# Performance work log

Hardware: AMD Instinct MI355X
Metric: run time of the kernel (lower is better)

## Reference

```python
import jax, jax.numpy as jnp
import numpy as np

D_MODEL = 1024
NHEAD = 16
HEAD_DIM = D_MODEL // NHEAD  # 64
SEQ = 2048
BATCH = 2


def setup_inputs() -> dict:
    key = jax.random.key(0)
    ks = jax.random.split(key, 11)
    s = 0.02  # weight init scale
    f32 = jnp.float32
    return {
        "query": jax.random.normal(ks[0], (SEQ, BATCH, D_MODEL), f32),
        "key": jax.random.normal(ks[1], (SEQ, BATCH, D_MODEL), f32),
        "value": jax.random.normal(ks[2], (SEQ, BATCH, D_MODEL), f32),
        "attn_mask": jnp.ones((SEQ, SEQ), jnp.int32),
        "Wq": jax.random.normal(ks[3], (D_MODEL, D_MODEL), f32) * s,
        "bq": jnp.zeros((D_MODEL,), f32),
        "Wk": jax.random.normal(ks[4], (D_MODEL, D_MODEL), f32) * s,
        "bk": jnp.zeros((D_MODEL,), f32),
        "Wv": jax.random.normal(ks[5], (D_MODEL, D_MODEL), f32) * s,
        "bv": jnp.zeros((D_MODEL,), f32),
        "Wo": jax.random.normal(ks[6], (D_MODEL, D_MODEL), f32) * s,
        "bo": jnp.zeros((D_MODEL,), f32),
    }


def reference(query, key, value, attn_mask, Wq, bq, Wk, bk, Wv, bv, Wo, bo):
    # query/key/value: [S, B, D] (seq-first, torch convention)
    S, B, D = query.shape
    H, Dh = NHEAD, D // NHEAD
    scale = 1.0 / np.float32(np.sqrt(Dh))

    def proj_heads(x, W, b):
        # Linear + split heads: [S,B,D] -> [H,B,S,Dh] (matches transpose(0,2))
        y = jnp.einsum('sbd,ed->sbe', x, W) + b
        return y.reshape(x.shape[0], B, H, Dh).transpose(2, 1, 0, 3)

    q = proj_heads(query, Wq, bq)   # [H,B,S,Dh]
    k = proj_heads(key, Wk, bk)     # [H,B,Sk,Dh]
    v = proj_heads(value, Wv, bv)   # [H,B,Sk,Dh]

    scores = jnp.einsum('hbqd,hbkd->hbqk', q, k) * scale  # [H,B,S,Sk]
    scores = jnp.where(attn_mask == 0, jnp.float32(-1e9), scores)
    attn_weights = jax.nn.softmax(scores, axis=-1)
    # dropout is identity in eval / p=0

    out = jnp.einsum('hbqk,hbkd->hbqd', attn_weights, v)  # [H,B,S,Dh]
    out = out.transpose(2, 1, 0, 3).reshape(S, B, D)
    out = jnp.einsum('sbd,ed->sbe', out, Wo) + bo
    return out, attn_weights
```

## Files before the change

kernel.cpp:

```cpp
#include <hip/hip_runtime.h>
#include <hip/hip_bf16.h>

#define DEVI __device__ __forceinline__

typedef __hip_bfloat16 bf16;
typedef __attribute__((ext_vector_type(8))) short bf16x8;
typedef __attribute__((ext_vector_type(4))) float f32x4;

constexpr int S  = 2048;
constexpr int B  = 2;
constexpr int D  = 1024;
constexpr int H  = 16;
constexpr int DH = 64;
constexpr int M  = S * B;
constexpr int K  = D;

DEVI f32x4 mfma16(bf16x8 a, bf16x8 b, f32x4 c) {
  return __builtin_amdgcn_mfma_f32_16x16x32_bf16(a, b, c, 0, 0, 0);
}

DEVI void gload16(const bf16* g, bf16* l) {
  __builtin_amdgcn_global_load_lds(
      (const __attribute__((address_space(1))) void*)g,
      (__attribute__((address_space(3))) void*)l, 16, 0, 0);
}

DEVI void cvt8_store(bf16* dst, float4 a, float4 b) {
  alignas(16) bf16 t[8];
  t[0] = __float2bfloat16(a.x); t[1] = __float2bfloat16(a.y);
  t[2] = __float2bfloat16(a.z); t[3] = __float2bfloat16(a.w);
  t[4] = __float2bfloat16(b.x); t[5] = __float2bfloat16(b.y);
  t[6] = __float2bfloat16(b.z); t[7] = __float2bfloat16(b.w);
  *(bf16x8*)dst = *(const bf16x8*)t;
}

__global__ __launch_bounds__(256)
void prep_k(const float* __restrict__ q, const float* __restrict__ k,
            const float* __restrict__ v,
            const float* __restrict__ Wq, const float* __restrict__ Wk,
            const float* __restrict__ Wv, const float* __restrict__ Wo,
            bf16* __restrict__ qb, bf16* __restrict__ kb, bf16* __restrict__ vb,
            bf16* __restrict__ wqb, bf16* __restrict__ wkb,
            bf16* __restrict__ wvb, bf16* __restrict__ wob) {
  int bid = blockIdx.x;
  const float* src; bf16* dst; int off;
  if      (bid < 2048) { src = q;  dst = qb;  off = bid; }
  else if (bid < 4096) { src = k;  dst = kb;  off = bid - 2048; }
  else if (bid < 6144) { src = v;  dst = vb;  off = bid - 4096; }
  else if (bid < 6656) { src = Wq; dst = wqb; off = bid - 6144; }
  else if (bid < 7168) { src = Wk; dst = wkb; off = bid - 6656; }
  else if (bid < 7680) { src = Wv; dst = wvb; off = bid - 7168; }
  else                 { src = Wo; dst = wob; off = bid - 7680; }
  size_t base = (size_t)off * 2048 + threadIdx.x * 8;
  float4 a = *(const float4*)&src[base];
  float4 c = *(const float4*)&src[base + 4];
  cvt8_store(&dst[base], a, c);
}

__global__ __launch_bounds__(256) void maskbits_k(const int* __restrict__ mask,
                                                  unsigned long long* __restrict__ bits) {
  int idx = blockIdx.x * 256 + threadIdx.x;
  int m = mask[idx];
  unsigned long long b = __ballot(m != 0);
  if ((threadIdx.x & 63) == 0) bits[idx >> 6] = b;
}

__global__ __launch_bounds__(64)
void rowfull_k(const unsigned long long* __restrict__ bits, unsigned* __restrict__ allq) {
  int g = blockIdx.x;
  int lane = threadIdx.x;
  bool ok = true;
  #pragma unroll
  for (int i = 0; i < 16; ++i)
    ok &= (bits[(size_t)g * 1024 + i * 64 + lane] == ~0ull);
  unsigned long long b = __ballot(ok);
  if (lane == 0) allq[g] = (b == ~0ull) ? 1u : 0u;
}

__global__ __launch_bounds__(256)
void gemm_qkv(const bf16* __restrict__ qb, const bf16* __restrict__ kb,
              const bf16* __restrict__ vb,
              const bf16* __restrict__ wqb, const bf16* __restrict__ wkb,
              const bf16* __restrict__ wvb,
              const float* __restrict__ bqp, const float* __restrict__ bkp,
              const float* __restrict__ bvp,
              bf16* __restrict__ qh, bf16* __restrict__ kh, bf16* __restrict__ vh) {
  __shared__ bf16 lA[128 * 64];
  __shared__ bf16 lB[128 * 64];

  const int z = blockIdx.z;
  const bf16* A     = (z == 0) ? qb  : (z == 1) ? kb  : vb;
  const bf16* W     = (z == 0) ? wqb : (z == 1) ? wkb : wvb;
  const float* bias = (z == 0) ? bqp : (z == 1) ? bkp : bvp;
  bf16* obf         = (z == 0) ? qh  : (z == 1) ? kh  : vh;

  const int tid  = threadIdx.x;
  const int lane = tid & 63;
  const int wave = tid >> 6;
  const int m0   = blockIdx.x * 128;
  const int n0   = blockIdx.y * 128;
  const int wm   = (wave >> 1) * 64;
  const int wn   = (wave & 1) * 64;
  const int lr   = lane & 15;
  const int lg   = lane >> 4;

  const int srow = wave * 32 + (lane >> 3);
  const int scol = (lane & 7) * 8;
  const bf16* gA = A + (size_t)(m0 + srow) * K + scol;
  const bf16* gB = W + (size_t)(n0 + srow) * K + scol;
  bf16* sA = &lA[srow * 64 + scol];
  bf16* sB = &lB[srow * 64 + scol];

  f32x4 acc[4][4] = {};

  for (int k0 = 0; k0 < K; k0 += 64) {
    __syncthreads();
    #pragma unroll
    for (int c = 0; c < 4; ++c) {
      gload16(gA + k0 + (size_t)c * 8 * K, sA + c * 8 * 64);
      gload16(gB + k0 + (size_t)c * 8 * K, sB + c * 8 * 64);
    }
    __syncthreads();

    bf16x8 af[4][2], bfv[4][2];
    #pragma unroll
    for (int f = 0; f < 4; ++f)
      #pragma unroll
      for (int kk = 0; kk < 2; ++kk) {
        af[f][kk]  = *(const bf16x8*)&lA[(wm + f * 16 + lr) * 64 + kk * 32 + lg * 8];
        bfv[f][kk] = *(const bf16x8*)&lB[(wn + f * 16 + lr) * 64 + kk * 32 + lg * 8];
      }
    #pragma unroll
    for (int kk = 0; kk < 2; ++kk)
      #pragma unroll
      for (int i = 0; i < 4; ++i)
        #pragma unroll
        for (int j = 0; j < 4; ++j)
          acc[i][j] = mfma16(af[i][kk], bfv[j][kk], acc[i][j]);
  }

  #pragma unroll
  for (int j = 0; j < 4; ++j) {
    int gcol = n0 + wn + j * 16 + lr;
    float bv = bias[gcol];
    int h = gcol >> 6, dh = gcol & 63;
    #pragma unroll
    for (int i = 0; i < 4; ++i) {
      #pragma unroll
      for (int r = 0; r < 4; ++r) {
        int grow = m0 + wm + i * 16 + lg * 4 + r;
        float v = acc[i][j][r] + bv;
        int s = grow >> 1, b = grow & 1;
        obf[(((size_t)(h * 2 + b) * S + s) * 64 + dh)] = __float2bfloat16(v);
      }
    }
  }
}

__global__ __launch_bounds__(256)
void transpose_v(const bf16* __restrict__ vh, bf16* __restrict__ vt) {
  __shared__ bf16 lt[64 * 72];
  const int hb = blockIdx.y;
  const int s0 = blockIdx.x * 64;
  const int tid = threadIdx.x;
  const int row = tid >> 3;
  const int c8  = (tid & 7) * 8;

  const bf16* src = vh + ((size_t)hb * S + s0) * 64;
  #pragma unroll
  for (int p = 0; p < 2; ++p) {
    int r = row + p * 32;
    *(float4*)&lt[r * 72 + c8] = *(const float4*)&src[(size_t)r * 64 + c8];
  }
  __syncthreads();

  bf16* dst = vt + (size_t)hb * DH * S + s0;
  #pragma unroll
  for (int p = 0; p < 2; ++p) {
    int dh = row + p * 32;
    alignas(16) bf16 tmp[8];
    #pragma unroll
    for (int kk = 0; kk < 8; ++kk) tmp[kk] = lt[(c8 + kk) * 72 + dh];
    *(bf16x8*)&dst[(size_t)dh * S + c8] = *(const bf16x8*)tmp;
  }
}

__global__ __launch_bounds__(256)
void gemm_out(const bf16* __restrict__ A, const bf16* __restrict__ W,
              const float* __restrict__ bias, float* __restrict__ of32) {
  __shared__ bf16 lA[128 * 64];
  __shared__ bf16 lB[128 * 64];

  const int tid  = threadIdx.x;
  const int lane = tid & 63;
  const int wave = tid >> 6;
  const int m0   = blockIdx.x * 128;
  const int n0   = blockIdx.y * 128;
  const int wm   = (wave >> 1) * 64;
  const int wn   = (wave & 1) * 64;
  const int lr   = lane & 15;
  const int lg   = lane >> 4;

  const int srow = wave * 32 + (lane >> 3);
  const int scol = (lane & 7) * 8;
  const bf16* gA = A + (size_t)(m0 + srow) * K + scol;
  const bf16* gB = W + (size_t)(n0 + srow) * K + scol;
  bf16* sA = &lA[srow * 64 + scol];
  bf16* sB = &lB[srow * 64 + scol];

  f32x4 acc[4][4] = {};

  for (int k0 = 0; k0 < K; k0 += 64) {
    __syncthreads();
    #pragma unroll
    for (int c = 0; c < 4; ++c) {
      gload16(gA + k0 + (size_t)c * 8 * K, sA + c * 8 * 64);
      gload16(gB + k0 + (size_t)c * 8 * K, sB + c * 8 * 64);
    }
    __syncthreads();

    bf16x8 af[4][2], bfv[4][2];
    #pragma unroll
    for (int f = 0; f < 4; ++f)
      #pragma unroll
      for (int kk = 0; kk < 2; ++kk) {
        af[f][kk]  = *(const bf16x8*)&lA[(wm + f * 16 + lr) * 64 + kk * 32 + lg * 8];
        bfv[f][kk] = *(const bf16x8*)&lB[(wn + f * 16 + lr) * 64 + kk * 32 + lg * 8];
      }
    #pragma unroll
    for (int kk = 0; kk < 2; ++kk)
      #pragma unroll
      for (int i = 0; i < 4; ++i)
        #pragma unroll
        for (int j = 0; j < 4; ++j)
          acc[i][j] = mfma16(af[i][kk], bfv[j][kk], acc[i][j]);
  }

  #pragma unroll
  for (int j = 0; j < 4; ++j) {
    int gcol = n0 + wn + j * 16 + lr;
    float bv = bias[gcol];
    #pragma unroll
    for (int i = 0; i < 4; ++i)
      #pragma unroll
      for (int r = 0; r < 4; ++r) {
        int grow = m0 + wm + i * 16 + lg * 4 + r;
        of32[(size_t)grow * D + gcol] = acc[i][j][r] + bv;
      }
  }
}


DEVI void stage_tile(const bf16* gbase, size_t gstride, int tid, bf16* lbuf) {
  #pragma unroll
  for (int i = 0; i < 2; ++i) {
    int slot = i * 256 + tid;
    int row  = slot >> 3;
    int colb = (slot & 7) * 16;
    int scolb = colb ^ ((row & 7) << 4);
    gload16(gbase + (size_t)row * gstride + (scolb >> 1), &lbuf[slot * 8]);
  }
}

DEVI bf16x8 frag_swz(const bf16* lbuf, int r, int colb) {
  int a = r * 128 + (colb ^ ((r & 7) << 4));
  return *(const bf16x8*)((const char*)lbuf + a);
}

__global__ __launch_bounds__(256)
void attn_k(const bf16* __restrict__ qh, const bf16* __restrict__ kh,
            const bf16* __restrict__ vt, const unsigned long long* __restrict__ mbits,
            const unsigned* __restrict__ allq,
            float* __restrict__ wout, bf16* __restrict__ aob) {
  __shared__ bf16 lK[2][64 * 64];
  __shared__ bf16 lV[2][64 * 64];
  __shared__ bf16 lW[4][16 * 40];

  const int tid = threadIdx.x, lane = tid & 63, wave = tid >> 6;
  const int hb = blockIdx.y;
  const int q0 = blockIdx.x * 64 + wave * 16;
  const bf16* Kb = kh + (size_t)hb * S * DH;
  const bf16* Vb = vt + (size_t)hb * DH * S;
  const bf16* Qb = qh + (size_t)hb * S * DH;
  const int lr = lane & 15, lg = lane >> 4;
  const float scale2 = 0.125f * 1.44269504089f;

  const bool fullmask = (allq[q0 >> 5] != 0u);

  bf16x8 qf[2];
  #pragma unroll
  for (int kk = 0; kk < 2; ++kk)
    qf[kk] = *(const bf16x8*)&Qb[(size_t)(q0 + lr) * DH + kk * 32 + lg * 8];

  float lrow[4] = {0.f, 0.f, 0.f, 0.f};

  stage_tile(Kb, DH, tid, lK[0]);
  for (int t = 0; t < 32; ++t) {
    int cur = t & 1;
    __syncthreads();
    if (t + 1 < 32) stage_tile(Kb + (size_t)(t + 1) * 64 * DH, DH, tid, lK[cur ^ 1]);

    f32x4 sa[4];
    #pragma unroll
    for (int c = 0; c < 4; ++c) {
      bf16x8 k0v = frag_swz(lK[cur], c * 16 + lr, lg * 16);
      bf16x8 k1v = frag_swz(lK[cur], c * 16 + lr, 64 + lg * 16);
      f32x4 z = {0.f, 0.f, 0.f, 0.f};
      z = mfma16(qf[0], k0v, z);
      sa[c] = mfma16(qf[1], k1v, z);
    }
    #pragma unroll
    for (int j = 0; j < 4; ++j) {
      float sv[4];
      #pragma unroll
      for (int c = 0; c < 4; ++c) sv[c] = sa[c][j] * scale2;
      if (!fullmask) {
        unsigned long long mw = mbits[(size_t)(q0 + lg * 4 + j) * 32 + t];
        #pragma unroll
        for (int c = 0; c < 4; ++c)
          sv[c] = ((mw >> (c * 16 + lr)) & 1ull) ? sv[c] : -1e9f;
      }
      lrow[j] += __builtin_amdgcn_exp2f(sv[0]) + __builtin_amdgcn_exp2f(sv[1])
               + __builtin_amdgcn_exp2f(sv[2]) + __builtin_amdgcn_exp2f(sv[3]);
    }
  }
  #pragma unroll
  for (int j = 0; j < 4; ++j) {
    float l = lrow[j];
    #pragma unroll
    for (int off = 1; off < 16; off <<= 1) l += __shfl_xor(l, off, 16);
    lrow[j] = 1.0f / l;
  }

  f32x4 oacc[4] = {};
  __syncthreads();
  stage_tile(Kb, DH, tid, lK[0]);
  stage_tile(Vb, S, tid, lV[0]);
  for (int t = 0; t < 32; ++t) {
    int cur = t & 1;
    __syncthreads();
    if (t + 1 < 32) {
      stage_tile(Kb + (size_t)(t + 1) * 64 * DH, DH, tid, lK[cur ^ 1]);
      stage_tile(Vb + (size_t)(t + 1) * 64, S, tid, lV[cur ^ 1]);
    }

    f32x4 sa[4];
    #pragma unroll
    for (int c = 0; c < 4; ++c) {
      bf16x8 k0v = frag_swz(lK[cur], c * 16 + lr, lg * 16);
      bf16x8 k1v = frag_swz(lK[cur], c * 16 + lr, 64 + lg * 16);
      f32x4 z = {0.f, 0.f, 0.f, 0.f};
      z = mfma16(qf[0], k0v, z);
      sa[c] = mfma16(qf[1], k1v, z);
    }

    #pragma unroll
    for (int u = 0; u < 2; ++u) {
      #pragma unroll
      for (int cc = 0; cc < 2; ++cc) {
        int c = u * 2 + cc;
        int cb = c * 16 + lr;
        #pragma unroll
        for (int j = 0; j < 4; ++j) {
          float sv = sa[c][j] * scale2;
          if (!fullmask) {
            unsigned long long mw = mbits[(size_t)(q0 + lg * 4 + j) * 32 + t];
            sv = ((mw >> cb) & 1ull) ? sv : -1e9f;
          }
          float w = __builtin_amdgcn_exp2f(sv) * lrow[j];
          int row = lg * 4 + j;
          wout[(size_t)(hb * S + q0 + row) * S + t * 64 + cb] = w;
          lW[wave][row * 40 + cc * 16 + lr] = __float2bfloat16(w);
        }
      }
      bf16x8 pa = *(const bf16x8*)&lW[wave][lr * 40 + lg * 8];
      #pragma unroll
      for (int nf = 0; nf < 4; ++nf) {
        bf16x8 vb = frag_swz(lV[cur], nf * 16 + lr, u * 64 + lg * 16);
        oacc[nf] = mfma16(pa, vb, oacc[nf]);
      }
    }
  }

  int h = hb >> 1, b = hb & 1;
  #pragma unroll
  for (int nf = 0; nf < 4; ++nf)
    #pragma unroll
    for (int r = 0; r < 4; ++r) {
      int sq = q0 + lg * 4 + r;
      int d  = h * 64 + nf * 16 + lr;
      aob[(size_t)(sq * 2 + b) * D + d] = __float2bfloat16(oacc[nf][r]);
    }
}

extern "C" void kernel_launch(void* const* d_in, const int* in_sizes, int n_in,
                              void* d_out, int out_size, void* d_ws, size_t ws_size,
                              hipStream_t stream) {
  const float* q    = (const float*)d_in[0];
  const float* k    = (const float*)d_in[1];
  const float* v    = (const float*)d_in[2];
  const int*   mask = (const int*)d_in[3];
  const float* Wq   = (const float*)d_in[4];
  const float* bq   = (const float*)d_in[5];
  const float* Wk   = (const float*)d_in[6];
  const float* bk   = (const float*)d_in[7];
  const float* Wv   = (const float*)d_in[8];
  const float* bv   = (const float*)d_in[9];
  const float* Wo   = (const float*)d_in[10];
  const float* bo   = (const float*)d_in[11];

  char* ws = (char*)d_ws;
  bf16* qh  = (bf16*)(ws);
  bf16* kh  = (bf16*)(ws + ((size_t)8  << 20));
  bf16* vt  = (bf16*)(ws + ((size_t)16 << 20));
  bf16* qbf = (bf16*)(ws + ((size_t)24 << 20));
  bf16* kbf = (bf16*)(ws + ((size_t)32 << 20));
  bf16* vbf = (bf16*)(ws + ((size_t)40 << 20));
  bf16* wqb = (bf16*)(ws + ((size_t)48 << 20));
  bf16* wkb = (bf16*)(ws + ((size_t)50 << 20));
  bf16* wvb = (bf16*)(ws + ((size_t)52 << 20));
  bf16* wob = (bf16*)(ws + ((size_t)54 << 20));
  unsigned long long* mbits =
      (unsigned long long*)(ws + ((size_t)56 << 20));
  unsigned* allq = (unsigned*)(ws + ((size_t)56 << 20) + (512 << 10));
  bf16* vh  = (bf16*)(ws + ((size_t)57 << 20));
  bf16* aob = qbf;

  float* outp = (float*)d_out;
  float* wout = outp + (size_t)M * D;

  prep_k<<<8192, 256, 0, stream>>>(q, k, v, Wq, Wk, Wv, Wo,
                                   qbf, kbf, vbf, wqb, wkb, wvb, wob);
  maskbits_k<<<dim3((S * S) / 256), 256, 0, stream>>>(mask, mbits);
  rowfull_k<<<64, 64, 0, stream>>>(mbits, allq);

  dim3 gq(M / 128, D / 128, 3);
  gemm_qkv<<<gq, 256, 0, stream>>>(qbf, kbf, vbf, wqb, wkb, wvb, bq, bk, bv,
                                   qh, kh, vh);

  dim3 gt(S / 64, H * B);
  transpose_v<<<gt, 256, 0, stream>>>(vh, vt);

  dim3 ga(S / 64, H * B);
  attn_k<<<ga, 256, 0, stream>>>(qh, kh, vt, mbits, allq, wout, aob);

  dim3 gg(M / 128, D / 128);
  gemm_out<<<gg, 256, 0, stream>>>(aob, wob, bo, outp);
}
```

Before: 312.0 us.

## Split attention pass-two into full-mask fast path with finer vmcnt barriers

Mask-fullness is now computed per 64-row query block instead of per 32 rows, so the whole block shares one uniform branch. In the full-mask case the second attention pass uses a specialised loop. It drops the per-element mask lookup and replaces __syncthreads with explicit s_waitcnt vmcnt plus s_barrier placed after compute, so the next tile's K/V loads can overlap the current tile's work. The hand-written vmcnt(16) count relies on the exact number of outstanding loads per stage, which is a correctness risk if that count differs.

```diff
diff --git a/kernel.cpp b/kernel.cpp
--- a/kernel.cpp
+++ b/kernel.cpp
@@ -71,8 +71,8 @@
   int lane = threadIdx.x;
   bool ok = true;
   #pragma unroll
-  for (int i = 0; i < 16; ++i)
-    ok &= (bits[(size_t)g * 1024 + i * 64 + lane] == ~0ull);
+  for (int i = 0; i < 32; ++i)
+    ok &= (bits[(size_t)g * 2048 + i * 64 + lane] == ~0ull);
   unsigned long long b = __ballot(ok);
   if (lane == 0) allq[g] = (b == ~0ull) ? 1u : 0u;
 }
@@ -285,7 +285,7 @@
   const int lr = lane & 15, lg = lane >> 4;
   const float scale2 = 0.125f * 1.44269504089f;
 
-  const bool fullmask = (allq[q0 >> 5] != 0u);
+  const bool fullmask = (allq[blockIdx.x] != 0u);
 
   bf16x8 qf[2];
   #pragma unroll
@@ -336,48 +336,99 @@
   __syncthreads();
   stage_tile(Kb, DH, tid, lK[0]);
   stage_tile(Vb, S, tid, lV[0]);
-  for (int t = 0; t < 32; ++t) {
-    int cur = t & 1;
-    __syncthreads();
-    if (t + 1 < 32) {
-      stage_tile(Kb + (size_t)(t + 1) * 64 * DH, DH, tid, lK[cur ^ 1]);
-      stage_tile(Vb + (size_t)(t + 1) * 64, S, tid, lV[cur ^ 1]);
-    }
-
-    f32x4 sa[4];
-    #pragma unroll
-    for (int c = 0; c < 4; ++c) {
-      bf16x8 k0v = frag_swz(lK[cur], c * 16 + lr, lg * 16);
-      bf16x8 k1v = frag_swz(lK[cur], c * 16 + lr, 64 + lg * 16);
-      f32x4 z = {0.f, 0.f, 0.f, 0.f};
-      z = mfma16(qf[0], k0v, z);
-      sa[c] = mfma16(qf[1], k1v, z);
-    }
-
-    #pragma unroll
-    for (int u = 0; u < 2; ++u) {
-      #pragma unroll
-      for (int cc = 0; cc < 2; ++cc) {
-        int c = u * 2 + cc;
-        int cb = c * 16 + lr;
-        #pragma unroll
-        for (int j = 0; j < 4; ++j) {
-          float sv = sa[c][j] * scale2;
-          if (!fullmask) {
+
+  if (fullmask) {
+    asm volatile("s_waitcnt vmcnt(0)" ::: "memory");
+    __builtin_amdgcn_sched_barrier(0);
+    __builtin_amdgcn_s_barrier();
+    for (int t = 0; t < 32; ++t) {
+      int cur = t & 1;
+      if (t + 1 < 32) {
+        stage_tile(Kb + (size_t)(t + 1) * 64 * DH, DH, tid, lK[cur ^ 1]);
+        stage_tile(Vb + (size_t)(t + 1) * 64, S, tid, lV[cur ^ 1]);
+      }
+      __builtin_amdgcn_sched_barrier(0);
+
+      f32x4 sa[4];
+      #pragma unroll
+      for (int c = 0; c < 4; ++c) {
+        bf16x8 k0v = frag_swz(lK[cur], c * 16 + lr, lg * 16);
+        bf16x8 k1v = frag_swz(lK[cur], c * 16 + lr, 64 + lg * 16);
+        f32x4 z = {0.f, 0.f, 0.f, 0.f};
+        z = mfma16(qf[0], k0v, z);
+        sa[c] = mfma16(qf[1], k1v, z);
+      }
+
+      #pragma unroll
+      for (int u = 0; u < 2; ++u) {
+        #pragma unroll
+        for (int cc = 0; cc < 2; ++cc) {
+          int c = u * 2 + cc;
+          int cb = c * 16 + lr;
+          #pragma unroll
+          for (int j = 0; j < 4; ++j) {
+            float w = __builtin_amdgcn_exp2f(sa[c][j] * scale2) * lrow[j];
+            int row = lg * 4 + j;
+            wout[(size_t)(hb * S + q0 + row) * S + t * 64 + cb] = w;
+            lW[wave][row * 40 + cc * 16 + lr] = __float2bfloat16(w);
+          }
+        }
+        bf16x8 pa = *(const bf16x8*)&lW[wave][lr * 40 + lg * 8];
+        #pragma unroll
+        for (int nf = 0; nf < 4; ++nf) {
+          bf16x8 vb = frag_swz(lV[cur], nf * 16 + lr, u * 64 + lg * 16);
+          oacc[nf] = mfma16(pa, vb, oacc[nf]);
+        }
+      }
+
+      if (t + 1 < 32) {
+        asm volatile("s_waitcnt vmcnt(16)" ::: "memory");
+        __builtin_amdgcn_sched_barrier(0);
+        __builtin_amdgcn_s_barrier();
+      }
+    }
+  } else {
+    for (int t = 0; t < 32; ++t) {
+      int cur = t & 1;
+      __syncthreads();
+      if (t + 1 < 32) {
+        stage_tile(Kb + (size_t)(t + 1) * 64 * DH, DH, tid, lK[cur ^ 1]);
+        stage_tile(Vb + (size_t)(t + 1) * 64, S, tid, lV[cur ^ 1]);
+      }
+
+      f32x4 sa[4];
+      #pragma unroll
+      for (int c = 0; c < 4; ++c) {
+        bf16x8 k0v = frag_swz(lK[cur], c * 16 + lr, lg * 16);
+        bf16x8 k1v = frag_swz(lK[cur], c * 16 + lr, 64 + lg * 16);
+        f32x4 z = {0.f, 0.f, 0.f, 0.f};
+        z = mfma16(qf[0], k0v, z);
+        sa[c] = mfma16(qf[1], k1v, z);
+      }
+
+      #pragma unroll
+      for (int u = 0; u < 2; ++u) {
+        #pragma unroll
+        for (int cc = 0; cc < 2; ++cc) {
+          int c = u * 2 + cc;
+          int cb = c * 16 + lr;
+          #pragma unroll
+          for (int j = 0; j < 4; ++j) {
+            float sv = sa[c][j] * scale2;
             unsigned long long mw = mbits[(size_t)(q0 + lg * 4 + j) * 32 + t];
             sv = ((mw >> cb) & 1ull) ? sv : -1e9f;
+            float w = __builtin_amdgcn_exp2f(sv) * lrow[j];
+            int row = lg * 4 + j;
+            wout[(size_t)(hb * S + q0 + row) * S + t * 64 + cb] = w;
+            lW[wave][row * 40 + cc * 16 + lr] = __float2bfloat16(w);
           }
-          float w = __builtin_amdgcn_exp2f(sv) * lrow[j];
-          int row = lg * 4 + j;
-          wout[(size_t)(hb * S + q0 + row) * S + t * 64 + cb] = w;
-          lW[wave][row * 40 + cc * 16 + lr] = __float2bfloat16(w);
         }
-      }
-      bf16x8 pa = *(const bf16x8*)&lW[wave][lr * 40 + lg * 8];
-      #pragma unroll
-      for (int nf = 0; nf < 4; ++nf) {
-        bf16x8 vb = frag_swz(lV[cur], nf * 16 + lr, u * 64 + lg * 16);
-        oacc[nf] = mfma16(pa, vb, oacc[nf]);
+        bf16x8 pa = *(const bf16x8*)&lW[wave][lr * 40 + lg * 8];
+        #pragma unroll
+        for (int nf = 0; nf < 4; ++nf) {
+          bf16x8 vb = frag_swz(lV[cur], nf * 16 + lr, u * 64 + lg * 16);
+          oacc[nf] = mfma16(pa, vb, oacc[nf]);
+        }
       }
     }
   }
@@ -432,7 +483,7 @@
   prep_k<<<8192, 256, 0, stream>>>(q, k, v, Wq, Wk, Wv, Wo,
                                    qbf, kbf, vbf, wqb, wkb, wvb, wob);
   maskbits_k<<<dim3((S * S) / 256), 256, 0, stream>>>(mask, mbits);
-  rowfull_k<<<64, 64, 0, stream>>>(mbits, allq);
+  rowfull_k<<<32, 64, 0, stream>>>(mbits, allq);
 
   dim3 gq(M / 128, D / 128, 3);
   gemm_qkv<<<gq, 256, 0, stream>>>(qbf, kbf, vbf, wqb, wkb, wvb, bq, bk, bv,
```

Result: slower. 353.1 us (+13.2%).

## Transpose score MFMA so each lane owns a query row for vectorized weight stores

Applied to the files above, without the earlier changes.

Swaps the MFMA operand order so the score tile is transposed: each lane now holds four consecutive key columns of a single query row. This lets the attention-weight output be written as float4 stores instead of scalar strided stores, and reduces mask-bit loads to one per lane per tile. Row sums become a per-lane accumulation plus two cross-lane shuffles. The full-mask check is regrouped to 64-row granularity per block, with rowfull_k launched on 32 groups to match.

```diff
diff --git a/kernel.cpp b/kernel.cpp
--- a/kernel.cpp
+++ b/kernel.cpp
@@ -71,8 +71,8 @@
   int lane = threadIdx.x;
   bool ok = true;
   #pragma unroll
-  for (int i = 0; i < 16; ++i)
-    ok &= (bits[(size_t)g * 1024 + i * 64 + lane] == ~0ull);
+  for (int i = 0; i < 32; ++i)
+    ok &= (bits[(size_t)g * 2048 + i * 64 + lane] == ~0ull);
   unsigned long long b = __ballot(ok);
   if (lane == 0) allq[g] = (b == ~0ull) ? 1u : 0u;
 }
@@ -285,14 +285,15 @@
   const int lr = lane & 15, lg = lane >> 4;
   const float scale2 = 0.125f * 1.44269504089f;
 
-  const bool fullmask = (allq[q0 >> 5] != 0u);
+  const bool fullmask = (allq[blockIdx.x] != 0u);
 
   bf16x8 qf[2];
   #pragma unroll
   for (int kk = 0; kk < 2; ++kk)
     qf[kk] = *(const bf16x8*)&Qb[(size_t)(q0 + lr) * DH + kk * 32 + lg * 8];
 
-  float lrow[4] = {0.f, 0.f, 0.f, 0.f};
+  const int myq = q0 + lr;
+  float lsum = 0.f;
 
   stage_tile(Kb, DH, tid, lK[0]);
   for (int t = 0; t < 32; ++t) {
@@ -306,31 +307,25 @@
       bf16x8 k0v = frag_swz(lK[cur], c * 16 + lr, lg * 16);
       bf16x8 k1v = frag_swz(lK[cur], c * 16 + lr, 64 + lg * 16);
       f32x4 z = {0.f, 0.f, 0.f, 0.f};
-      z = mfma16(qf[0], k0v, z);
-      sa[c] = mfma16(qf[1], k1v, z);
-    }
-    #pragma unroll
-    for (int j = 0; j < 4; ++j) {
-      float sv[4];
-      #pragma unroll
-      for (int c = 0; c < 4; ++c) sv[c] = sa[c][j] * scale2;
-      if (!fullmask) {
-        unsigned long long mw = mbits[(size_t)(q0 + lg * 4 + j) * 32 + t];
-        #pragma unroll
-        for (int c = 0; c < 4; ++c)
-          sv[c] = ((mw >> (c * 16 + lr)) & 1ull) ? sv[c] : -1e9f;
-      }
-      lrow[j] += __builtin_amdgcn_exp2f(sv[0]) + __builtin_amdgcn_exp2f(sv[1])
-               + __builtin_amdgcn_exp2f(sv[2]) + __builtin_amdgcn_exp2f(sv[3]);
-    }
-  }
-  #pragma unroll
-  for (int j = 0; j < 4; ++j) {
-    float l = lrow[j];
-    #pragma unroll
-    for (int off = 1; off < 16; off <<= 1) l += __shfl_xor(l, off, 16);
-    lrow[j] = 1.0f / l;
-  }
+      z = mfma16(k0v, qf[0], z);
+      sa[c] = mfma16(k1v, qf[1], z);
+    }
+    unsigned long long mw = 0;
+    if (!fullmask) mw = mbits[(size_t)myq * 32 + t];
+    #pragma unroll
+    for (int c = 0; c < 4; ++c) {
+      #pragma unroll
+      for (int j = 0; j < 4; ++j) {
+        float sv = sa[c][j] * scale2;
+        if (!fullmask)
+          sv = ((mw >> (c * 16 + lg * 4 + j)) & 1ull) ? sv : -1e9f;
+        lsum += __builtin_amdgcn_exp2f(sv);
+      }
+    }
+  }
+  lsum += __shfl_xor(lsum, 16);
+  lsum += __shfl_xor(lsum, 32);
+  const float linv = 1.0f / lsum;
 
   f32x4 oacc[4] = {};
   __syncthreads();
@@ -350,28 +345,31 @@
       bf16x8 k0v = frag_swz(lK[cur], c * 16 + lr, lg * 16);
       bf16x8 k1v = frag_swz(lK[cur], c * 16 + lr, 64 + lg * 16);
       f32x4 z = {0.f, 0.f, 0.f, 0.f};
-      z = mfma16(qf[0], k0v, z);
-      sa[c] = mfma16(qf[1], k1v, z);
-    }
+      z = mfma16(k0v, qf[0], z);
+      sa[c] = mfma16(k1v, qf[1], z);
+    }
+    unsigned long long mw = 0;
+    if (!fullmask) mw = mbits[(size_t)myq * 32 + t];
+
+    float* wrow = &wout[(size_t)(hb * S + myq) * S + t * 64];
 
     #pragma unroll
     for (int u = 0; u < 2; ++u) {
       #pragma unroll
       for (int cc = 0; cc < 2; ++cc) {
         int c = u * 2 + cc;
-        int cb = c * 16 + lr;
+        float4 wv;
+        float* wp = &wv.x;
         #pragma unroll
         for (int j = 0; j < 4; ++j) {
           float sv = sa[c][j] * scale2;
-          if (!fullmask) {
-            unsigned long long mw = mbits[(size_t)(q0 + lg * 4 + j) * 32 + t];
-            sv = ((mw >> cb) & 1ull) ? sv : -1e9f;
-          }
-          float w = __builtin_amdgcn_exp2f(sv) * lrow[j];
-          int row = lg * 4 + j;
-          wout[(size_t)(hb * S + q0 + row) * S + t * 64 + cb] = w;
-          lW[wave][row * 40 + cc * 16 + lr] = __float2bfloat16(w);
+          if (!fullmask)
+            sv = ((mw >> (c * 16 + lg * 4 + j)) & 1ull) ? sv : -1e9f;
+          float w2 = __builtin_amdgcn_exp2f(sv) * linv;
+          wp[j] = w2;
+          lW[wave][lr * 40 + cc * 16 + lg * 4 + j] = __float2bfloat16(w2);
         }
+        *(float4*)&wrow[c * 16 + lg * 4] = wv;
       }
       bf16x8 pa = *(const bf16x8*)&lW[wave][lr * 40 + lg * 8];
       #pragma unroll
@@ -432,7 +430,7 @@
   prep_k<<<8192, 256, 0, stream>>>(q, k, v, Wq, Wk, Wv, Wo,
                                    qbf, kbf, vbf, wqb, wkb, wvb, wob);
   maskbits_k<<<dim3((S * S) / 256), 256, 0, stream>>>(mask, mbits);
-  rowfull_k<<<64, 64, 0, stream>>>(mbits, allq);
+  rowfull_k<<<32, 64, 0, stream>>>(mbits, allq);
 
   dim3 gq(M / 128, D / 128, 3);
   gemm_qkv<<<gq, 256, 0, stream>>>(qbf, kbf, vbf, wqb, wkb, wvb, bq, bk, bv,
```

Result: slower. 377.1 us (+20.9%).

## Move softmax row-sum pass out of attention into a separate tiled QK kernel

Applied to the files above, without the earlier changes.

The first pass of the attention kernel, which recomputed QK^T to get softmax denominators, is replaced by a standalone qk_sums kernel. It computes 128x128 score tiles over a full (q-tile, k-tile, head) grid and writes per-tile partial row sums, and make_linv reduces those into reciprocal denominators. The attention kernel then runs only its second pass, which keeps it from being serialized across 32 K tiles just for sums. Mask-full granularity changes to 64-row groups to match. In exchange it adds two launches and a partial-sum buffer round trip through global memory.

```diff
diff --git a/kernel.cpp b/kernel.cpp
--- a/kernel.cpp
+++ b/kernel.cpp
@@ -71,8 +71,8 @@
   int lane = threadIdx.x;
   bool ok = true;
   #pragma unroll
-  for (int i = 0; i < 16; ++i)
-    ok &= (bits[(size_t)g * 1024 + i * 64 + lane] == ~0ull);
+  for (int i = 0; i < 32; ++i)
+    ok &= (bits[(size_t)g * 2048 + i * 64 + lane] == ~0ull);
   unsigned long long b = __ballot(ok);
   if (lane == 0) allq[g] = (b == ~0ull) ? 1u : 0u;
 }
@@ -250,6 +250,91 @@
   }
 }
 
+__global__ __launch_bounds__(256)
+void qk_sums(const bf16* __restrict__ qh, const bf16* __restrict__ kh,
+             const unsigned long long* __restrict__ mbits,
+             const unsigned* __restrict__ allq, float* __restrict__ lpart) {
+  __shared__ bf16 lA[128 * 64];
+  __shared__ bf16 lB[128 * 64];
+
+  const int tid = threadIdx.x, lane = tid & 63, wave = tid >> 6;
+  const int hb = blockIdx.z;
+  const int m0 = blockIdx.x * 128;
+  const int n0 = blockIdx.y * 128;
+  const bf16* A  = qh + (size_t)hb * S * DH;
+  const bf16* Bk = kh + (size_t)hb * S * DH;
+  const int wm = (wave >> 1) * 64, wn = (wave & 1) * 64;
+  const int lr = lane & 15, lg = lane >> 4;
+  const float scale2 = 0.125f * 1.44269504089f;
+
+  const bool fullmask = (allq[2 * blockIdx.x] & allq[2 * blockIdx.x + 1]) != 0u;
+
+  #pragma unroll
+  for (int i = 0; i < 4; ++i) {
+    int slot = i * 256 + tid;
+    int row = slot >> 3, c8 = (slot & 7) * 8;
+    gload16(A  + (size_t)(m0 + row) * DH + c8, &lA[slot * 8]);
+    gload16(Bk + (size_t)(n0 + row) * DH + c8, &lB[slot * 8]);
+  }
+  __syncthreads();
+
+  f32x4 acc[4][4] = {};
+  bf16x8 af[4][2], bfv[4][2];
+  #pragma unroll
+  for (int f = 0; f < 4; ++f)
+    #pragma unroll
+    for (int kk = 0; kk < 2; ++kk) {
+      af[f][kk]  = *(const bf16x8*)&lA[(wm + f * 16 + lr) * 64 + kk * 32 + lg * 8];
+      bfv[f][kk] = *(const bf16x8*)&lB[(wn + f * 16 + lr) * 64 + kk * 32 + lg * 8];
+    }
+  #pragma unroll
+  for (int kk = 0; kk < 2; ++kk)
+    #pragma unroll
+    for (int i = 0; i < 4; ++i)
+      #pragma unroll
+      for (int j = 0; j < 4; ++j)
+        acc[i][j] = mfma16(af[i][kk], bfv[j][kk], acc[i][j]);
+
+  __syncthreads();
+  float* lps = (float*)lA;
+  const int wordi = (n0 + wn) >> 6;
+
+  #pragma unroll
+  for (int i = 0; i < 4; ++i) {
+    #pragma unroll
+    for (int r = 0; r < 4; ++r) {
+      int rowl = wm + i * 16 + lg * 4 + r;
+      unsigned long long mw = ~0ull;
+      if (!fullmask) mw = mbits[(size_t)(m0 + rowl) * 32 + wordi];
+      float part = 0.f;
+      #pragma unroll
+      for (int j = 0; j < 4; ++j) {
+        float sv = acc[i][j][r] * scale2;
+        if (!fullmask) sv = ((mw >> (j * 16 + lr)) & 1ull) ? sv : -1e9f;
+        part += __builtin_amdgcn_exp2f(sv);
+      }
+      #pragma unroll
+      for (int off = 1; off < 16; off <<= 1) part += __shfl_xor(part, off, 16);
+      if (lr == 0) lps[(wave & 1) * 128 + rowl] = part;
+    }
+  }
+  __syncthreads();
+  if (tid < 128) {
+    float s = lps[tid] + lps[128 + tid];
+    lpart[((size_t)(hb * 16 + blockIdx.y) * S) + m0 + tid] = s;
+  }
+}
+
+__global__ __launch_bounds__(256)
+void make_linv(const float* __restrict__ lpart, float* __restrict__ linv) {
+  int t = blockIdx.x * 256 + threadIdx.x;
+  int hb = t >> 11, row = t & 2047;
+  float s = 0.f;
+  #pragma unroll
+  for (int y = 0; y < 16; ++y) s += lpart[((size_t)(hb * 16 + y) * S) + row];
+  linv[t] = 1.0f / s;
+}
+
 
 DEVI void stage_tile(const bf16* gbase, size_t gstride, int tid, bf16* lbuf) {
   #pragma unroll
@@ -270,7 +355,7 @@
 __global__ __launch_bounds__(256)
 void attn_k(const bf16* __restrict__ qh, const bf16* __restrict__ kh,
             const bf16* __restrict__ vt, const unsigned long long* __restrict__ mbits,
-            const unsigned* __restrict__ allq,
+            const unsigned* __restrict__ allq, const float* __restrict__ linv,
             float* __restrict__ wout, bf16* __restrict__ aob) {
   __shared__ bf16 lK[2][64 * 64];
   __shared__ bf16 lV[2][64 * 64];
@@ -285,55 +370,19 @@
   const int lr = lane & 15, lg = lane >> 4;
   const float scale2 = 0.125f * 1.44269504089f;
 
-  const bool fullmask = (allq[q0 >> 5] != 0u);
+  const bool fullmask = (allq[blockIdx.x] != 0u);
 
   bf16x8 qf[2];
   #pragma unroll
   for (int kk = 0; kk < 2; ++kk)
     qf[kk] = *(const bf16x8*)&Qb[(size_t)(q0 + lr) * DH + kk * 32 + lg * 8];
 
-  float lrow[4] = {0.f, 0.f, 0.f, 0.f};
-
-  stage_tile(Kb, DH, tid, lK[0]);
-  for (int t = 0; t < 32; ++t) {
-    int cur = t & 1;
-    __syncthreads();
-    if (t + 1 < 32) stage_tile(Kb + (size_t)(t + 1) * 64 * DH, DH, tid, lK[cur ^ 1]);
-
-    f32x4 sa[4];
-    #pragma unroll
-    for (int c = 0; c < 4; ++c) {
-      bf16x8 k0v = frag_swz(lK[cur], c * 16 + lr, lg * 16);
-      bf16x8 k1v = frag_swz(lK[cur], c * 16 + lr, 64 + lg * 16);
-      f32x4 z = {0.f, 0.f, 0.f, 0.f};
-      z = mfma16(qf[0], k0v, z);
-      sa[c] = mfma16(qf[1], k1v, z);
-    }
-    #pragma unroll
-    for (int j = 0; j < 4; ++j) {
-      float sv[4];
-      #pragma unroll
-      for (int c = 0; c < 4; ++c) sv[c] = sa[c][j] * scale2;
-      if (!fullmask) {
-        unsigned long long mw = mbits[(size_t)(q0 + lg * 4 + j) * 32 + t];
-        #pragma unroll
-        for (int c = 0; c < 4; ++c)
-          sv[c] = ((mw >> (c * 16 + lr)) & 1ull) ? sv[c] : -1e9f;
-      }
-      lrow[j] += __builtin_amdgcn_exp2f(sv[0]) + __builtin_amdgcn_exp2f(sv[1])
-               + __builtin_amdgcn_exp2f(sv[2]) + __builtin_amdgcn_exp2f(sv[3]);
-    }
-  }
-  #pragma unroll
-  for (int j = 0; j < 4; ++j) {
-    float l = lrow[j];
-    #pragma unroll
-    for (int off = 1; off < 16; off <<= 1) l += __shfl_xor(l, off, 16);
-    lrow[j] = 1.0f / l;
-  }
+  float linvv[4];
+  #pragma unroll
+  for (int j = 0; j < 4; ++j)
+    linvv[j] = linv[hb * S + q0 + lg * 4 + j];
 
   f32x4 oacc[4] = {};
-  __syncthreads();
   stage_tile(Kb, DH, tid, lK[0]);
   stage_tile(Vb, S, tid, lV[0]);
   for (int t = 0; t < 32; ++t) {
@@ -367,10 +416,10 @@
             unsigned long long mw = mbits[(size_t)(q0 + lg * 4 + j) * 32 + t];
             sv = ((mw >> cb) & 1ull) ? sv : -1e9f;
           }
-          float w = __builtin_amdgcn_exp2f(sv) * lrow[j];
+          float w2 = __builtin_amdgcn_exp2f(sv) * linvv[j];
           int row = lg * 4 + j;
-          wout[(size_t)(hb * S + q0 + row) * S + t * 64 + cb] = w;
-          lW[wave][row * 40 + cc * 16 + lr] = __float2bfloat16(w);
+          wout[(size_t)(hb * S + q0 + row) * S + t * 64 + cb] = w2;
+          lW[wave][row * 40 + cc * 16 + lr] = __float2bfloat16(w2);
         }
       }
       bf16x8 pa = *(const bf16x8*)&lW[wave][lr * 40 + lg * 8];
@@ -424,6 +473,8 @@
       (unsigned long long*)(ws + ((size_t)56 << 20));
   unsigned* allq = (unsigned*)(ws + ((size_t)56 << 20) + (512 << 10));
   bf16* vh  = (bf16*)(ws + ((size_t)57 << 20));
+  float* lpart = (float*)(ws + ((size_t)65 << 20));
+  float* linv  = (float*)(ws + ((size_t)69 << 20));
   bf16* aob = qbf;
 
   float* outp = (float*)d_out;
@@ -432,7 +483,7 @@
   prep_k<<<8192, 256, 0, stream>>>(q, k, v, Wq, Wk, Wv, Wo,
                                    qbf, kbf, vbf, wqb, wkb, wvb, wob);
   maskbits_k<<<dim3((S * S) / 256), 256, 0, stream>>>(mask, mbits);
-  rowfull_k<<<64, 64, 0, stream>>>(mbits, allq);
+  rowfull_k<<<32, 64, 0, stream>>>(mbits, allq);
 
   dim3 gq(M / 128, D / 128, 3);
   gemm_qkv<<<gq, 256, 0, stream>>>(qbf, kbf, vbf, wqb, wkb, wvb, bq, bk, bv,
@@ -441,8 +492,12 @@
   dim3 gt(S / 64, H * B);
   transpose_v<<<gt, 256, 0, stream>>>(vh, vt);
 
+  dim3 gs(S / 128, S / 128, H * B);
+  qk_sums<<<gs, 256, 0, stream>>>(qh, kh, mbits, allq, lpart);
+  make_linv<<<(H * B * S) / 256, 256, 0, stream>>>(lpart, linv);
+
   dim3 ga(S / 64, H * B);
-  attn_k<<<ga, 256, 0, stream>>>(qh, kh, vt, mbits, allq, wout, aob);
+  attn_k<<<ga, 256, 0, stream>>>(qh, kh, vt, mbits, allq, linv, wout, aob);
 
   dim3 gg(M / 128, D / 128);
   gemm_out<<<gg, 256, 0, stream>>>(aob, wob, bo, outp);
```

New measurement: 370.0 us. 18.6% more time.
